# Kernel tuning notes

Measured on AMD Instinct MI355X. Metric: run time of the kernel, lower is better.

## Reference

```python
import jax, jax.numpy as jnp
import numpy as np

B, L, E, H = 128, 256, 256, 512


def setup_inputs() -> dict:
    key = jax.random.key(0)
    ks = jax.random.split(key, 16)
    s = 0.02
    return {
        "embedded_inputs": jax.random.normal(ks[0], (B, L, E), jnp.float32),
        "decoder_input": jax.random.normal(ks[1], (B, E), jnp.float32),
        "dec_h": jax.random.normal(ks[2], (B, H), jnp.float32),
        "dec_c": jax.random.normal(ks[3], (B, H), jnp.float32),
        "context": jax.random.normal(ks[4], (B, L, H), jnp.float32),
        # Decoder params
        "W_i2h": jax.random.normal(ks[5], (4 * H, E), jnp.float32) * s,
        "b_i2h": jnp.zeros((4 * H,), jnp.float32),
        "W_h2h": jax.random.normal(ks[6], (4 * H, H), jnp.float32) * s,
        "b_h2h": jnp.zeros((4 * H,), jnp.float32),
        "W_out": jax.random.normal(ks[7], (H, 2 * H), jnp.float32) * s,
        "b_out": jnp.zeros((H,), jnp.float32),
        # Attention params
        "W_inp": jax.random.normal(ks[8], (H, H), jnp.float32) * s,
        "b_inp": jnp.zeros((H,), jnp.float32),
        "W_ctx": jax.random.normal(ks[9], (H, H), jnp.float32) * s,  # Conv1d(k=1) kernel squeezed
        "b_ctx": jnp.zeros((H,), jnp.float32),
        "V": jax.random.uniform(ks[10], (H,), jnp.float32, -1.0, 1.0),
    }


def reference(embedded_inputs, decoder_input, dec_h, dec_c, context,
              W_i2h, b_i2h, W_h2h, b_h2h, W_out, b_out,
              W_inp, b_inp, W_ctx, b_ctx, V):
    # Precompute projected context: Conv1d(k=1) == per-position linear. ctx: [B, H, L]
    ctx = jnp.einsum("blh,gh->bgl", context, W_ctx) + b_ctx[None, :, None]
    seq_len = embedded_inputs.shape[1]

    def step(carry, _):
        x, h, c, mask = carry
        gates = x @ W_i2h.T + b_i2h + h @ W_h2h.T + b_h2h
        i, f, g, o = jnp.split(gates, 4, axis=1)
        c_t = jax.nn.sigmoid(f) * c + jax.nn.sigmoid(i) * jnp.tanh(g)
        h_t = jax.nn.sigmoid(o) * jnp.tanh(c_t)
        # attention
        inp = h_t @ W_inp.T + b_inp                              # [B, H]
        scores = jnp.einsum("h,bhl->bl", V, jnp.tanh(inp[:, :, None] + ctx))
        att = jnp.where(mask == 0, -jnp.inf, scores)
        alpha = jax.nn.softmax(att, axis=-1)                     # [B, L]
        hidden = jnp.einsum("bhl,bl->bh", ctx, alpha)
        h_new = jnp.tanh(jnp.concatenate([hidden, h_t], axis=1) @ W_out.T + b_out)
        # pointer selection
        idx = jnp.argmax(alpha * mask, axis=1)                   # [B]
        one_hot = jax.nn.one_hot(idx, seq_len, dtype=mask.dtype)
        mask_new = mask * (1.0 - one_hot)
        next_x = jnp.take_along_axis(embedded_inputs, idx[:, None, None], axis=1)[:, 0, :]
        return (next_x, h_new, c_t, mask_new), (alpha, idx)

    mask0 = jnp.ones((embedded_inputs.shape[0], seq_len), jnp.float32)
    (x_f, h_f, c_f, _), (alphas, ptrs) = jax.lax.scan(
        step, (decoder_input, dec_h, dec_c, mask0), None, length=seq_len)
    outputs = jnp.transpose(alphas, (1, 0, 2))   # [B, L, L]
    pointers = jnp.transpose(ptrs, (1, 0))       # [B, L]
    return outputs, pointers, h_f, c_f
```

## Files before the change

### kernel.cpp

```cpp
#include <hip/hip_runtime.h>

#define B 128
#define L 256
#define E 256
#define H 512
#define NBLK 256
#define NTHR 512

typedef float f4 __attribute__((ext_vector_type(4)));

#define WS_CTX 0u
#define WS_HT  18874368u
#define WS_HH  18939904u
#define WS_HID 19005440u
#define WS_INP 19071232u
#define WS_XT  19136768u
#define WS_FLG 19169536u

#define OUT_ALPHA 0u
#define OUT_PTR   8388608u
#define OUT_H     8421376u
#define OUT_C     8486912u

#define L2E 1.4426950408889634f

__device__ __forceinline__ float fast_rcp(float x) { return __builtin_amdgcn_rcpf(x); }

__device__ __forceinline__ float ftanh(float x) {
  float e = exp2f(x * (2.0f * L2E));
  return 1.0f - 2.0f * fast_rcp(e + 1.0f);
}
__device__ __forceinline__ float fsig(float x) {
  float e = exp2f(-x * L2E);
  return fast_rcp(1.0f + e);
}

#define CLD1(v0, p0)                                                          \
  asm volatile("global_load_dwordx4 %0, %1, off sc0 sc1\n\t"                  \
               "s_waitcnt vmcnt(0)"                                           \
               : "=&v"(v0) : "v"(p0) : "memory")

#define CLD2(va, pa)                                                          \
  asm volatile("global_load_dwordx4 %0, %2, off sc0 sc1\n\t"                  \
               "global_load_dwordx4 %1, %3, off sc0 sc1\n\t"                  \
               "s_waitcnt vmcnt(0)"                                           \
               : "=&v"(va[0]), "=&v"(va[1])                                   \
               : "v"(pa[0]), "v"(pa[1]) : "memory")

#define CLD4(va, pa)                                                          \
  asm volatile("global_load_dwordx4 %0, %4, off sc0 sc1\n\t"                  \
               "global_load_dwordx4 %1, %5, off sc0 sc1\n\t"                  \
               "global_load_dwordx4 %2, %6, off sc0 sc1\n\t"                  \
               "global_load_dwordx4 %3, %7, off sc0 sc1\n\t"                  \
               "s_waitcnt vmcnt(0)"                                           \
               : "=&v"(va[0]), "=&v"(va[1]), "=&v"(va[2]), "=&v"(va[3])       \
               : "v"(pa[0]), "v"(pa[1]), "v"(pa[2]), "v"(pa[3]) : "memory")

#define CLD6(va, pa)                                                          \
  asm volatile("global_load_dwordx4 %0, %6, off sc0 sc1\n\t"                  \
               "global_load_dwordx4 %1, %7, off sc0 sc1\n\t"                  \
               "global_load_dwordx4 %2, %8, off sc0 sc1\n\t"                  \
               "global_load_dwordx4 %3, %9, off sc0 sc1\n\t"                  \
               "global_load_dwordx4 %4, %10, off sc0 sc1\n\t"                 \
               "global_load_dwordx4 %5, %11, off sc0 sc1\n\t"                 \
               "s_waitcnt vmcnt(0)"                                           \
               : "=&v"(va[0]), "=&v"(va[1]), "=&v"(va[2]), "=&v"(va[3]),      \
                 "=&v"(va[4]), "=&v"(va[5])                                   \
               : "v"(pa[0]), "v"(pa[1]), "v"(pa[2]), "v"(pa[3]),              \
                 "v"(pa[4]), "v"(pa[5]) : "memory")

#define CST4_1(p0, v0)                                                        \
  asm volatile("global_store_dwordx4 %0, %1, off sc0 sc1\n\t"                 \
               "s_waitcnt expcnt(0)"                                          \
               :: "v"(p0), "v"(v0) : "memory")

__device__ __forceinline__ void gbar(unsigned* flags, unsigned tgt) {
  asm volatile("s_waitcnt vmcnt(0) lgkmcnt(0) expcnt(0)" ::: "memory");
  __syncthreads();
  if (threadIdx.x == 0) {
    unsigned* p = flags + blockIdx.x;
    asm volatile("global_store_dword %0, %1, off sc0 sc1" :: "v"(p), "v"(tgt) : "memory");
  }
  if (blockIdx.x == 0) {
    if (threadIdx.x < 64) {
      const unsigned* fp = flags + threadIdx.x * 4;
      for (;;) {
        unsigned f0, f1, f2, f3;
        asm volatile("global_load_dwordx4 v[20:23], %4, off sc0 sc1\n\t"
                     "s_waitcnt vmcnt(0)\n\t"
                     "v_mov_b32 %0, v20\n\t"
                     "v_mov_b32 %1, v21\n\t"
                     "v_mov_b32 %2, v22\n\t"
                     "v_mov_b32 %3, v23"
                     : "=v"(f0), "=v"(f1), "=v"(f2), "=v"(f3)
                     : "v"(fp) : "memory", "v20", "v21", "v22", "v23");
        bool ok = (f0 >= tgt) && (f1 >= tgt) && (f2 >= tgt) && (f3 >= tgt);
        if (__all(ok)) break;
        __builtin_amdgcn_s_sleep(1);
      }
    }
    __syncthreads();
    if (threadIdx.x == 0) {
      unsigned* gp = flags + 320;
      asm volatile("global_store_dword %0, %1, off sc0 sc1" :: "v"(gp), "v"(tgt) : "memory");
    }
  } else {
    if (threadIdx.x == 0) {
      const unsigned* gp = flags + 320;
      for (;;) {
        unsigned g;
        asm volatile("global_load_dword %0, %1, off sc0 sc1\n\ts_waitcnt vmcnt(0)"
                     : "=&v"(g) : "v"(gp) : "memory");
        if (g >= tgt) break;
        __builtin_amdgcn_s_sleep(4);
      }
    }
  }
  __syncthreads();
}

__global__ __launch_bounds__(256) void k_ctx(const float* __restrict__ context,
                                             const float* __restrict__ Wc,
                                             const float* __restrict__ bc,
                                             float* __restrict__ ws) {
  __shared__ float a_lds[64][33];
  __shared__ float b_lds[32][68];
  int t = threadIdx.x;
  int m0 = blockIdx.x * 64;
  int n0 = blockIdx.y * 64;
  int tx = t & 15, ty = t >> 4;
  float acc[4][4] = {};
  for (int kc = 0; kc < 16; ++kc) {
    int k0 = kc * 32;
    __syncthreads();
#pragma unroll
    for (int i = 0; i < 2; ++i) {
      int f40 = t + i * 256;
      int mm = f40 >> 3;
      int k4 = (f40 & 7) * 4;
      float4 v = *(const float4*)&context[(size_t)(m0 + mm) * H + k0 + k4];
      a_lds[mm][k4] = v.x; a_lds[mm][k4 + 1] = v.y; a_lds[mm][k4 + 2] = v.z; a_lds[mm][k4 + 3] = v.w;
    }
#pragma unroll
    for (int i = 0; i < 2; ++i) {
      int f40 = t + i * 256;
      int nn = f40 >> 3;
      int k4 = (f40 & 7) * 4;
      float4 v = *(const float4*)&Wc[(size_t)(n0 + nn) * H + k0 + k4];
      b_lds[k4][nn] = v.x; b_lds[k4 + 1][nn] = v.y; b_lds[k4 + 2][nn] = v.z; b_lds[k4 + 3][nn] = v.w;
    }
    __syncthreads();
#pragma unroll
    for (int kk = 0; kk < 32; ++kk) {
      float4 bv = *(const float4*)&b_lds[kk][tx * 4];
      float a0 = a_lds[ty * 4 + 0][kk], a1 = a_lds[ty * 4 + 1][kk];
      float a2 = a_lds[ty * 4 + 2][kk], a3 = a_lds[ty * 4 + 3][kk];
      acc[0][0] += a0 * bv.x; acc[0][1] += a0 * bv.y; acc[0][2] += a0 * bv.z; acc[0][3] += a0 * bv.w;
      acc[1][0] += a1 * bv.x; acc[1][1] += a1 * bv.y; acc[1][2] += a1 * bv.z; acc[1][3] += a1 * bv.w;
      acc[2][0] += a2 * bv.x; acc[2][1] += a2 * bv.y; acc[2][2] += a2 * bv.z; acc[2][3] += a2 * bv.w;
      acc[3][0] += a3 * bv.x; acc[3][1] += a3 * bv.y; acc[3][2] += a3 * bv.z; acc[3][3] += a3 * bv.w;
    }
  }
  float b0v = bc[n0 + tx * 4], b1v = bc[n0 + tx * 4 + 1], b2v = bc[n0 + tx * 4 + 2], b3v = bc[n0 + tx * 4 + 3];
#pragma unroll
  for (int i = 0; i < 4; ++i) {
    size_t o = WS_CTX + (size_t)(m0 + ty * 4 + i) * H + n0 + tx * 4;
    float4 v; v.x = acc[i][0] + b0v; v.y = acc[i][1] + b1v; v.z = acc[i][2] + b2v; v.w = acc[i][3] + b3v;
    *(float4*)&ws[o] = v;
  }
}

__global__ __launch_bounds__(256) void k_init(const float* __restrict__ dec_h,
                                              const float* __restrict__ dec_in,
                                              float* __restrict__ ws) {
  int flat = blockIdx.x * 256 + threadIdx.x;
  if (flat < 65536) {
    ws[WS_HH + flat] = dec_h[flat];
  } else if (flat < 98304) {
    ws[WS_XT + (flat - 65536)] = dec_in[flat - 65536];
  } else if (flat < 98816) {
    ((unsigned*)(ws + WS_FLG))[flat - 98304] = 0u;
  }
}

__global__ __launch_bounds__(512, 1) void k_main(
    const float* __restrict__ Wi2h, const float* __restrict__ bi2h,
    const float* __restrict__ Wh2h, const float* __restrict__ bh2h,
    const float* __restrict__ Wout, const float* __restrict__ bout,
    const float* __restrict__ Winp, const float* __restrict__ binp,
    const float* __restrict__ Vv,   const float* __restrict__ emb,
    const float* __restrict__ dec_c,
    float* __restrict__ ws,         float* __restrict__ out) {
  __shared__ float s_act[13504];
  __shared__ float s_maskP[256];
  __shared__ float s_mw[8], s_dw[8];
  __shared__ float s_red[4];
  __shared__ int   s_redi[4];
  __shared__ int   s_wc[4], s_wb[4];
  __shared__ int   s_mi, s_cnt;

  unsigned* flags = (unsigned*)(ws + WS_FLG);
  const int bid = blockIdx.x;
  const int t = threadIdx.x;
  const int wv = t >> 6, ln = t & 63;
  unsigned tgt = 0;

  float creg = 0.f;

  if (bid < 128 && t < 256) s_maskP[t] = 1.0f;
  __syncthreads();

  for (int step = 0; step < L; ++step) {
    {
      const int jt = bid >> 3, bt = bid & 7;
      const int u0 = jt * 16, b0 = bt * 16;
      float* sact = s_act;
      float* sg   = s_act + 12352;
      f4 va[6]; const float* pa[6]; int sb[6], sq[6];
#pragma unroll
      for (int it = 0; it < 6; ++it) {
        unsigned c = (unsigned)(t + it * 512);
        int bl = (int)(c / 192u);
        int kq = (int)(c - (unsigned)bl * 192u);
        int kg = kq * 4;
        sb[it] = bl; sq[it] = kq;
        pa[it] = (kg < 256) ? ws + WS_XT + (size_t)(b0 + bl) * 256 + kg
                            : ws + WS_HH + (size_t)(b0 + bl) * 512 + (kg - 256);
      }
      CLD6(va, pa);
      __builtin_amdgcn_sched_barrier(0);
#pragma unroll
      for (int it = 0; it < 6; ++it) *(f4*)&sact[sb[it] * 772 + sq[it] * 4] = va[it];
      __syncthreads();

      const int jj = t >> 4, bb = t & 15;
      const int g = jj >> 3, up = (jj & 7) * 2;
      const int r0 = g * 512 + u0 + up;
      float a0 = 0.f, a1 = 0.f;
      {
        const float* w0 = Wi2h + (size_t)r0 * 256;
        const float* w1 = w0 + 256;
        const float* sa = sact + bb * 772;
#pragma unroll 8
        for (int k4 = 0; k4 < 64; ++k4) {
          float4 x = *(const float4*)&sa[k4 * 4];
          float4 p = *(const float4*)&w0[k4 * 4];
          float4 q = *(const float4*)&w1[k4 * 4];
          a0 += p.x * x.x + p.y * x.y + p.z * x.z + p.w * x.w;
          a1 += q.x * x.x + q.y * x.y + q.z * x.z + q.w * x.w;
        }
        const float* v0 = Wh2h + (size_t)r0 * 512;
        const float* v1 = v0 + 512;
        const float* shh = sa + 256;
#pragma unroll 8
        for (int k4 = 0; k4 < 128; ++k4) {
          float4 x = *(const float4*)&shh[k4 * 4];
          float4 p = *(const float4*)&v0[k4 * 4];
          float4 q = *(const float4*)&v1[k4 * 4];
          a0 += p.x * x.x + p.y * x.y + p.z * x.z + p.w * x.w;
          a1 += q.x * x.x + q.y * x.y + q.z * x.z + q.w * x.w;
        }
      }
      sg[(g * 16 + up) * 17 + bb]     = a0;
      sg[(g * 16 + up + 1) * 17 + bb] = a1;
      __syncthreads();
      if (t < 256) {
        const int uu = t >> 4, b2 = t & 15;
        const int j0 = u0 + uu;
        float si_ = sg[(     uu) * 17 + b2] + bi2h[       j0] + bh2h[       j0];
        float sf_ = sg[(16 + uu) * 17 + b2] + bi2h[ 512 + j0] + bh2h[ 512 + j0];
        float sg_ = sg[(32 + uu) * 17 + b2] + bi2h[1024 + j0] + bh2h[1024 + j0];
        float so_ = sg[(48 + uu) * 17 + b2] + bi2h[1536 + j0] + bh2h[1536 + j0];
        if (step == 0) creg = dec_c[(size_t)(b0 + b2) * 512 + j0];
        float cn = fsig(sf_) * creg + fsig(si_) * ftanh(sg_);
        creg = cn;
        float htv = fsig(so_) * ftanh(cn);
        s_act[b2 * 17 + uu] = htv;
        if (step == L - 1) out[OUT_C + (size_t)(b0 + b2) * 512 + j0] = cn;
      }
      __syncthreads();
      if (t < 64) {
        const int b2 = t >> 2, q = t & 3;
        f4 hv;
        hv[0] = s_act[b2 * 17 + q * 4 + 0];
        hv[1] = s_act[b2 * 17 + q * 4 + 1];
        hv[2] = s_act[b2 * 17 + q * 4 + 2];
        hv[3] = s_act[b2 * 17 + q * 4 + 3];
        float* hp = ws + WS_HT + (size_t)(b0 + b2) * 512 + u0 + q * 4;
        CST4_1(hp, hv);
      }
    }
    ++tgt; gbar(flags, tgt);

    {
      const int gt = bid >> 4, bt = bid & 15;
      const int g0 = gt * 32, b0 = bt * 8;
      float* si = s_act;
      float* stmp = s_act + 4128;
      f4 va[2]; const float* pa[2];
#pragma unroll
      for (int it = 0; it < 2; ++it) {
        int c = t + it * 512;
        int bl = c >> 7, kq = c & 127;
        pa[it] = ws + WS_HT + (size_t)(b0 + bl) * 512 + kq * 4;
      }
      CLD2(va, pa);
      __builtin_amdgcn_sched_barrier(0);
#pragma unroll
      for (int it = 0; it < 2; ++it) {
        int c = t + it * 512;
        int bl = c >> 7, kq = c & 127;
        *(f4*)&si[bl * 516 + kq * 4] = va[it];
      }
      __syncthreads();
      if (t < 256) {
        const int gl = t >> 3, bb = t & 7;
        const float* w = Winp + (size_t)(g0 + gl) * 512;
        const float* sa = si + bb * 516;
        float acc = 0.f;
#pragma unroll 8
        for (int k4 = 0; k4 < 128; ++k4) {
          float4 ww = *(const float4*)&w[k4 * 4];
          float4 xx = *(const float4*)&sa[k4 * 4];
          acc += ww.x * xx.x + ww.y * xx.y + ww.z * xx.z + ww.w * xx.w;
        }
        stmp[bb * 33 + gl] = acc + binp[g0 + gl];
      }
      __syncthreads();
      if (t < 64) {
        const int bb = t >> 3, q = t & 7;
        f4 v;
        v[0] = stmp[bb * 33 + q * 4 + 0];
        v[1] = stmp[bb * 33 + q * 4 + 1];
        v[2] = stmp[bb * 33 + q * 4 + 2];
        v[3] = stmp[bb * 33 + q * 4 + 3];
        float* p = ws + WS_INP + (size_t)(b0 + bb) * 512 + g0 + q * 4;
        CST4_1(p, v);
      }
    }
    ++tgt; gbar(flags, tgt);

    if (bid < 128) {
      const int b = bid;
      float* s_inp  = s_act;
      float* s_sc   = s_act + 512;
      int*   s_li   = (int*)(s_act + 768);
      float* s_hidp = s_act + 1024;
      float* s_out  = s_act + 5120;
      if (t < 128) {
        f4 v;
        const float* p = ws + WS_INP + (size_t)b * 512 + t * 4;
        CLD1(v, p);
        *(f4*)&s_inp[t * 4] = v;
      }
      __syncthreads();
      const int d0 = ln * 8;
      float inp8[8], v8[8];
#pragma unroll
      for (int i = 0; i < 8; ++i) { inp8[i] = s_inp[d0 + i]; v8[i] = Vv[d0 + i]; }
      bool validl = (t < 256) && (s_maskP[t] != 0.f);
      unsigned long long bal = __ballot(validl);
      if (t < 256 && (t & 63) == 0) s_wc[t >> 6] = (int)__popcll(bal);
      __syncthreads();
      if (t == 0) {
        int base = 0;
#pragma unroll
        for (int i = 0; i < 4; ++i) { s_wb[i] = base; base += s_wc[i]; }
        s_cnt = base;
      }
      __syncthreads();
      if (validl) {
        int idx = s_wb[t >> 6] + (int)__popcll(bal & ((1ull << (t & 63)) - 1ull));
        s_li[idx] = t;
      }
      __syncthreads();
      const int cnt = s_cnt;
      float m = -INFINITY, den = 0.f;
      float hid[8] = {0, 0, 0, 0, 0, 0, 0, 0};
      {
        int slot = wv;
        int l = 0; f4 c0 = {0, 0, 0, 0}, c1 = c0;
        if (slot < cnt) {
          l = s_li[slot];
          const float* cp = ws + WS_CTX + ((size_t)(b * 256 + l) * 512) + d0;
          c0 = *(const f4*)cp; c1 = *(const f4*)(cp + 4);
        }
        while (slot < cnt) {
          const int nslot = slot + 8;
          int nl = 0; f4 n0 = {0, 0, 0, 0}, n1 = n0;
          if (nslot < cnt) {
            nl = s_li[nslot];
            const float* np = ws + WS_CTX + ((size_t)(b * 256 + nl) * 512) + d0;
            n0 = *(const f4*)np; n1 = *(const f4*)(np + 4);
          }
          float part = v8[0] * ftanh(inp8[0] + c0[0]) + v8[1] * ftanh(inp8[1] + c0[1])
                     + v8[2] * ftanh(inp8[2] + c0[2]) + v8[3] * ftanh(inp8[3] + c0[3])
                     + v8[4] * ftanh(inp8[4] + c1[0]) + v8[5] * ftanh(inp8[5] + c1[1])
                     + v8[6] * ftanh(inp8[6] + c1[2]) + v8[7] * ftanh(inp8[7] + c1[3]);
#pragma unroll
          for (int off = 32; off > 0; off >>= 1) part += __shfl_xor(part, off);
          if (ln == 0) s_sc[l] = part;
          float mn = fmaxf(m, part);
          float scale = exp2f((m - mn) * L2E);
          float e = exp2f((part - mn) * L2E);
          den = den * scale + e;
          hid[0] = hid[0] * scale + e * c0[0]; hid[1] = hid[1] * scale + e * c0[1];
          hid[2] = hid[2] * scale + e * c0[2]; hid[3] = hid[3] * scale + e * c0[3];
          hid[4] = hid[4] * scale + e * c1[0]; hid[5] = hid[5] * scale + e * c1[1];
          hid[6] = hid[6] * scale + e * c1[2]; hid[7] = hid[7] * scale + e * c1[3];
          m = mn;
          c0 = n0; c1 = n1; l = nl; slot = nslot;
        }
      }
      if (ln == 0) { s_mw[wv] = m; s_dw[wv] = den; }
      __syncthreads();
      float M = s_mw[0];
#pragma unroll
      for (int w = 1; w < 8; ++w) M = fmaxf(M, s_mw[w]);
      float D = 0.f;
#pragma unroll
      for (int w = 0; w < 8; ++w) D += s_dw[w] * exp2f((s_mw[w] - M) * L2E);
      float fac = exp2f((m - M) * L2E);
#pragma unroll
      for (int i = 0; i < 8; ++i) s_hidp[wv * 512 + d0 + i] = hid[i] * fac;
      __syncthreads();
      const float rD = 1.0f / D;
      {
        float hs = 0.f;
#pragma unroll
        for (int w = 0; w < 8; ++w) hs += s_hidp[w * 512 + t];
        s_out[t] = hs * rD;
      }
      float sc = 0.f; bool valid = false;
      if (t < 256) {
        valid = (s_maskP[t] != 0.f);
        sc = s_sc[t];
        float alpha = valid ? exp2f((sc - M) * L2E) * rD : 0.f;
        out[OUT_ALPHA + ((size_t)b * 256 + step) * 256 + t] = alpha;
        float bs = valid ? sc : -INFINITY;
        int bi = t;
#pragma unroll
        for (int off = 32; off > 0; off >>= 1) {
          float os = __shfl_down(bs, off);
          int oi = __shfl_down(bi, off);
          if (os > bs || (os == bs && oi < bi)) { bs = os; bi = oi; }
        }
        if ((t & 63) == 0) { s_red[t >> 6] = bs; s_redi[t >> 6] = bi; }
      }
      __syncthreads();
      if (t == 0) {
        float mm = s_red[0]; int mi = s_redi[0];
#pragma unroll
        for (int w = 1; w < 4; ++w) {
          if (s_red[w] > mm || (s_red[w] == mm && s_redi[w] < mi)) { mm = s_red[w]; mi = s_redi[w]; }
        }
        s_mi = mi;
      }
      __syncthreads();
      const int mi = s_mi;
      if (t < 128) {
        f4 hv = *(const f4*)&s_out[t * 4];
        float* hp = ws + WS_HID + (size_t)b * 512 + t * 4;
        CST4_1(hp, hv);
      }
      if (t < 64) {
        float4 xv = *(const float4*)&emb[((size_t)b * 256 + mi) * 256 + t * 4];
        f4 xq; xq[0] = xv.x; xq[1] = xv.y; xq[2] = xv.z; xq[3] = xv.w;
        float* xp = ws + WS_XT + (size_t)b * 256 + t * 4;
        CST4_1(xp, xq);
      }
      if (t == 0) {
        out[OUT_PTR + (size_t)b * 256 + step] = (float)mi;
        s_maskP[mi] = 0.f;
      }
    }
    ++tgt; gbar(flags, tgt);

    {
      const int rt = bid >> 4, bt = bid & 15;
      const int r0 = rt * 32, b0 = bt * 8;
      float* sh = s_act;
      float* stmp = s_act + 8224;
      f4 va[4]; const float* pa[4];
#pragma unroll
      for (int it = 0; it < 4; ++it) {
        int c = t + it * 512;
        int bl = c >> 8, kq = c & 255;
        int kg = kq * 4;
        pa[it] = (kg < 512) ? ws + WS_HID + (size_t)(b0 + bl) * 512 + kg
                            : ws + WS_HT + (size_t)(b0 + bl) * 512 + (kg - 512);
      }
      CLD4(va, pa);
      __builtin_amdgcn_sched_barrier(0);
#pragma unroll
      for (int it = 0; it < 4; ++it) {
        int c = t + it * 512;
        int bl = c >> 8, kq = c & 255;
        *(f4*)&sh[bl * 1028 + kq * 4] = va[it];
      }
      __syncthreads();
      if (t < 256) {
        const int rl = t >> 3, bb = t & 7;
        const float* w = Wout + (size_t)(r0 + rl) * 1024;
        const float* sa = sh + bb * 1028;
        float acc = 0.f;
#pragma unroll 8
        for (int k4 = 0; k4 < 256; ++k4) {
          float4 ww = *(const float4*)&w[k4 * 4];
          float4 xx = *(const float4*)&sa[k4 * 4];
          acc += ww.x * xx.x + ww.y * xx.y + ww.z * xx.z + ww.w * xx.w;
        }
        float h = ftanh(acc + bout[r0 + rl]);
        stmp[bb * 33 + rl] = h;
        if (step == L - 1) out[OUT_H + (size_t)(b0 + bb) * 512 + r0 + rl] = h;
      }
      __syncthreads();
      if (t < 64) {
        const int bb = t >> 3, q = t & 7;
        f4 v;
        v[0] = stmp[bb * 33 + q * 4 + 0];
        v[1] = stmp[bb * 33 + q * 4 + 1];
        v[2] = stmp[bb * 33 + q * 4 + 2];
        v[3] = stmp[bb * 33 + q * 4 + 3];
        float* p = ws + WS_HH + (size_t)(b0 + bb) * 512 + r0 + q * 4;
        CST4_1(p, v);
      }
    }
    ++tgt; gbar(flags, tgt);
  }
}

extern "C" void kernel_launch(void* const* d_in, const int* in_sizes, int n_in,
                              void* d_out, int out_size, void* d_ws, size_t ws_size,
                              hipStream_t stream) {
  (void)in_sizes; (void)n_in; (void)out_size; (void)ws_size;
  const float* emb    = (const float*)d_in[0];
  const float* dec_in = (const float*)d_in[1];
  const float* dec_h  = (const float*)d_in[2];
  const float* dec_c  = (const float*)d_in[3];
  const float* ctx_in = (const float*)d_in[4];
  const float* W_i2h  = (const float*)d_in[5];
  const float* b_i2h  = (const float*)d_in[6];
  const float* W_h2h  = (const float*)d_in[7];
  const float* b_h2h  = (const float*)d_in[8];
  const float* W_out  = (const float*)d_in[9];
  const float* b_out  = (const float*)d_in[10];
  const float* W_inp  = (const float*)d_in[11];
  const float* b_inp  = (const float*)d_in[12];
  const float* W_ctx  = (const float*)d_in[13];
  const float* b_ctx  = (const float*)d_in[14];
  const float* Vv     = (const float*)d_in[15];
  float* out = (float*)d_out;
  float* ws  = (float*)d_ws;

  k_ctx<<<dim3(512, 8), 256, 0, stream>>>(ctx_in, W_ctx, b_ctx, ws);
  k_init<<<386, 256, 0, stream>>>(dec_h, dec_in, ws);
  k_main<<<NBLK, NTHR, 0, stream>>>(W_i2h, b_i2h, W_h2h, b_h2h, W_out, b_out,
                                    W_inp, b_inp, Vv, emb, dec_c, ws, out);
}
```

Measured before the change: 18.97 ms.

## Pad barrier flags, remap block tiles per XCD, and unroll attention loop by four

Each block's grid-barrier flag now sits on its own padded slot, and the release flag is replicated eight times so waiters spread across copies selected by blockIdx&7. The waiter sleep interval is also shortened. Block-to-tile mappings in the three GEMM phases are permuted so blocks sharing bid&7 (likely the same XCD) work on neighbouring weight rows. The attention loop now handles four context positions per iteration with nontemporal prefetched loads and a batched online-softmax update, which cuts shuffle-reduction serialization but raises register pressure.

Result: faster. 16.53 ms (-12.9%).

```diff
diff --git a/kernel.cpp b/kernel.cpp
--- a/kernel.cpp
+++ b/kernel.cpp
@@ -78,41 +78,42 @@
   asm volatile("s_waitcnt vmcnt(0) lgkmcnt(0) expcnt(0)" ::: "memory");
   __syncthreads();
   if (threadIdx.x == 0) {
-    unsigned* p = flags + blockIdx.x;
+    unsigned* p = flags + blockIdx.x * 16;
     asm volatile("global_store_dword %0, %1, off sc0 sc1" :: "v"(p), "v"(tgt) : "memory");
   }
   if (blockIdx.x == 0) {
     if (threadIdx.x < 64) {
-      const unsigned* fp = flags + threadIdx.x * 4;
+      const unsigned* p0 = flags + (threadIdx.x * 4 + 0) * 16;
+      const unsigned* p1 = flags + (threadIdx.x * 4 + 1) * 16;
+      const unsigned* p2 = flags + (threadIdx.x * 4 + 2) * 16;
+      const unsigned* p3 = flags + (threadIdx.x * 4 + 3) * 16;
       for (;;) {
         unsigned f0, f1, f2, f3;
-        asm volatile("global_load_dwordx4 v[20:23], %4, off sc0 sc1\n\t"
-                     "s_waitcnt vmcnt(0)\n\t"
-                     "v_mov_b32 %0, v20\n\t"
-                     "v_mov_b32 %1, v21\n\t"
-                     "v_mov_b32 %2, v22\n\t"
-                     "v_mov_b32 %3, v23"
-                     : "=v"(f0), "=v"(f1), "=v"(f2), "=v"(f3)
-                     : "v"(fp) : "memory", "v20", "v21", "v22", "v23");
-        bool ok = (f0 >= tgt) && (f1 >= tgt) && (f2 >= tgt) && (f3 >= tgt);
-        if (__all(ok)) break;
+        asm volatile("global_load_dword %0, %4, off sc0 sc1\n\t"
+                     "global_load_dword %1, %5, off sc0 sc1\n\t"
+                     "global_load_dword %2, %6, off sc0 sc1\n\t"
+                     "global_load_dword %3, %7, off sc0 sc1\n\t"
+                     "s_waitcnt vmcnt(0)"
+                     : "=&v"(f0), "=&v"(f1), "=&v"(f2), "=&v"(f3)
+                     : "v"(p0), "v"(p1), "v"(p2), "v"(p3) : "memory");
+        if (__all(f0 >= tgt && f1 >= tgt && f2 >= tgt && f3 >= tgt)) break;
         __builtin_amdgcn_s_sleep(1);
       }
     }
     __syncthreads();
-    if (threadIdx.x == 0) {
-      unsigned* gp = flags + 320;
+    if (threadIdx.x < 8) {
+      unsigned* gp = flags + 4096 + threadIdx.x * 16;
       asm volatile("global_store_dword %0, %1, off sc0 sc1" :: "v"(gp), "v"(tgt) : "memory");
     }
   } else {
     if (threadIdx.x == 0) {
-      const unsigned* gp = flags + 320;
+      const unsigned* gp = flags + 4096 + (blockIdx.x & 7) * 16;
       for (;;) {
         unsigned g;
         asm volatile("global_load_dword %0, %1, off sc0 sc1\n\ts_waitcnt vmcnt(0)"
                      : "=&v"(g) : "v"(gp) : "memory");
         if (g >= tgt) break;
-        __builtin_amdgcn_s_sleep(4);
+        __builtin_amdgcn_s_sleep(2);
       }
     }
   }
@@ -178,7 +179,7 @@
     ws[WS_HH + flat] = dec_h[flat];
   } else if (flat < 98304) {
     ws[WS_XT + (flat - 65536)] = dec_in[flat - 65536];
-  } else if (flat < 98816) {
+  } else if (flat < 102528) {
     ((unsigned*)(ws + WS_FLG))[flat - 98304] = 0u;
   }
 }
@@ -212,7 +213,8 @@
 
   for (int step = 0; step < L; ++step) {
     {
-      const int jt = bid >> 3, bt = bid & 7;
+      const int jt = (bid & 7) * 4 + ((bid >> 3) & 3);
+      const int bt = bid >> 5;
       const int u0 = jt * 16, b0 = bt * 16;
       float* sact = s_act;
       float* sg   = s_act + 12352;
@@ -293,7 +295,8 @@
     ++tgt; gbar(flags, tgt);
 
     {
-      const int gt = bid >> 4, bt = bid & 15;
+      const int gt = (bid & 7) * 2 + ((bid >> 3) & 1);
+      const int bt = bid >> 4;
       const int g0 = gt * 32, b0 = bt * 8;
       float* si = s_act;
       float* stmp = s_act + 4128;
@@ -378,38 +381,102 @@
       float m = -INFINITY, den = 0.f;
       float hid[8] = {0, 0, 0, 0, 0, 0, 0, 0};
       {
-        int slot = wv;
-        int l = 0; f4 c0 = {0, 0, 0, 0}, c1 = c0;
-        if (slot < cnt) {
-          l = s_li[slot];
-          const float* cp = ws + WS_CTX + ((size_t)(b * 256 + l) * 512) + d0;
-          c0 = *(const f4*)cp; c1 = *(const f4*)(cp + 4);
-        }
-        while (slot < cnt) {
-          const int nslot = slot + 8;
-          int nl = 0; f4 n0 = {0, 0, 0, 0}, n1 = n0;
-          if (nslot < cnt) {
-            nl = s_li[nslot];
-            const float* np = ws + WS_CTX + ((size_t)(b * 256 + nl) * 512) + d0;
-            n0 = *(const f4*)np; n1 = *(const f4*)(np + 4);
+        f4 cur0a, cur0b, cur1a, cur1b, cur2a, cur2b, cur3a, cur3b;
+        int l0i, l1i, l2i, l3i;
+        int base = wv * 4;
+        {
+          int s0 = base, s1 = base + 1, s2 = base + 2, s3 = base + 3;
+          int a = (s0 < cnt) ? s_li[s0] : 0;  l0i = (s0 < cnt) ? a : -1;
+          int bb2 = (s1 < cnt) ? s_li[s1] : 0; l1i = (s1 < cnt) ? bb2 : -1;
+          int c = (s2 < cnt) ? s_li[s2] : 0;  l2i = (s2 < cnt) ? c : -1;
+          int d = (s3 < cnt) ? s_li[s3] : 0;  l3i = (s3 < cnt) ? d : -1;
+          const f4* p0 = (const f4*)(ws + WS_CTX + ((size_t)(b * 256 + a) * 512) + d0);
+          const f4* p1 = (const f4*)(ws + WS_CTX + ((size_t)(b * 256 + bb2) * 512) + d0);
+          const f4* p2 = (const f4*)(ws + WS_CTX + ((size_t)(b * 256 + c) * 512) + d0);
+          const f4* p3 = (const f4*)(ws + WS_CTX + ((size_t)(b * 256 + d) * 512) + d0);
+          cur0a = __builtin_nontemporal_load(p0); cur0b = __builtin_nontemporal_load(p0 + 1);
+          cur1a = __builtin_nontemporal_load(p1); cur1b = __builtin_nontemporal_load(p1 + 1);
+          cur2a = __builtin_nontemporal_load(p2); cur2b = __builtin_nontemporal_load(p2 + 1);
+          cur3a = __builtin_nontemporal_load(p3); cur3b = __builtin_nontemporal_load(p3 + 1);
+        }
+        for (; base < cnt; base += 32) {
+          f4 n0a, n0b, n1a, n1b, n2a, n2b, n3a, n3b;
+          int nl0, nl1, nl2, nl3;
+          {
+            int s0 = base + 32, s1 = base + 33, s2 = base + 34, s3 = base + 35;
+            int a = (s0 < cnt) ? s_li[s0] : 0;  nl0 = (s0 < cnt) ? a : -1;
+            int bb2 = (s1 < cnt) ? s_li[s1] : 0; nl1 = (s1 < cnt) ? bb2 : -1;
+            int c = (s2 < cnt) ? s_li[s2] : 0;  nl2 = (s2 < cnt) ? c : -1;
+            int d = (s3 < cnt) ? s_li[s3] : 0;  nl3 = (s3 < cnt) ? d : -1;
+            const f4* p0 = (const f4*)(ws + WS_CTX + ((size_t)(b * 256 + a) * 512) + d0);
+            const f4* p1 = (const f4*)(ws + WS_CTX + ((size_t)(b * 256 + bb2) * 512) + d0);
+            const f4* p2 = (const f4*)(ws + WS_CTX + ((size_t)(b * 256 + c) * 512) + d0);
+            const f4* p3 = (const f4*)(ws + WS_CTX + ((size_t)(b * 256 + d) * 512) + d0);
+            n0a = __builtin_nontemporal_load(p0); n0b = __builtin_nontemporal_load(p0 + 1);
+            n1a = __builtin_nontemporal_load(p1); n1b = __builtin_nontemporal_load(p1 + 1);
+            n2a = __builtin_nontemporal_load(p2); n2b = __builtin_nontemporal_load(p2 + 1);
+            n3a = __builtin_nontemporal_load(p3); n3b = __builtin_nontemporal_load(p3 + 1);
           }
-          float part = v8[0] * ftanh(inp8[0] + c0[0]) + v8[1] * ftanh(inp8[1] + c0[1])
-                     + v8[2] * ftanh(inp8[2] + c0[2]) + v8[3] * ftanh(inp8[3] + c0[3])
-                     + v8[4] * ftanh(inp8[4] + c1[0]) + v8[5] * ftanh(inp8[5] + c1[1])
-                     + v8[6] * ftanh(inp8[6] + c1[2]) + v8[7] * ftanh(inp8[7] + c1[3]);
-#pragma unroll
-          for (int off = 32; off > 0; off >>= 1) part += __shfl_xor(part, off);
-          if (ln == 0) s_sc[l] = part;
-          float mn = fmaxf(m, part);
+          float sv0, sv1, sv2, sv3;
+          {
+            float part = v8[0] * ftanh(inp8[0] + cur0a[0]) + v8[1] * ftanh(inp8[1] + cur0a[1])
+                       + v8[2] * ftanh(inp8[2] + cur0a[2]) + v8[3] * ftanh(inp8[3] + cur0a[3])
+                       + v8[4] * ftanh(inp8[4] + cur0b[0]) + v8[5] * ftanh(inp8[5] + cur0b[1])
+                       + v8[6] * ftanh(inp8[6] + cur0b[2]) + v8[7] * ftanh(inp8[7] + cur0b[3]);
+#pragma unroll
+            for (int off = 32; off > 0; off >>= 1) part += __shfl_xor(part, off);
+            if (l0i >= 0 && ln == 0) s_sc[l0i] = part;
+            sv0 = (l0i >= 0) ? part : -INFINITY;
+          }
+          {
+            float part = v8[0] * ftanh(inp8[0] + cur1a[0]) + v8[1] * ftanh(inp8[1] + cur1a[1])
+                       + v8[2] * ftanh(inp8[2] + cur1a[2]) + v8[3] * ftanh(inp8[3] + cur1a[3])
+                       + v8[4] * ftanh(inp8[4] + cur1b[0]) + v8[5] * ftanh(inp8[5] + cur1b[1])
+                       + v8[6] * ftanh(inp8[6] + cur1b[2]) + v8[7] * ftanh(inp8[7] + cur1b[3]);
+#pragma unroll
+            for (int off = 32; off > 0; off >>= 1) part += __shfl_xor(part, off);
+            if (l1i >= 0 && ln == 0) s_sc[l1i] = part;
+            sv1 = (l1i >= 0) ? part : -INFINITY;
+          }
+          {
+            float part = v8[0] * ftanh(inp8[0] + cur2a[0]) + v8[1] * ftanh(inp8[1] + cur2a[1])
+                       + v8[2] * ftanh(inp8[2] + cur2a[2]) + v8[3] * ftanh(inp8[3] + cur2a[3])
+                       + v8[4] * ftanh(inp8[4] + cur2b[0]) + v8[5] * ftanh(inp8[5] + cur2b[1])
+                       + v8[6] * ftanh(inp8[6] + cur2b[2]) + v8[7] * ftanh(inp8[7] + cur2b[3]);
+#pragma unroll
+            for (int off = 32; off > 0; off >>= 1) part += __shfl_xor(part, off);
+            if (l2i >= 0 && ln == 0) s_sc[l2i] = part;
+            sv2 = (l2i >= 0) ? part : -INFINITY;
+          }
+          {
+            float part = v8[0] * ftanh(inp8[0] + cur3a[0]) + v8[1] * ftanh(inp8[1] + cur3a[1])
+                       + v8[2] * ftanh(inp8[2] + cur3a[2]) + v8[3] * ftanh(inp8[3] + cur3a[3])
+                       + v8[4] * ftanh(inp8[4] + cur3b[0]) + v8[5] * ftanh(inp8[5] + cur3b[1])
+                       + v8[6] * ftanh(inp8[6] + cur3b[2]) + v8[7] * ftanh(inp8[7] + cur3b[3]);
+#pragma unroll
+            for (int off = 32; off > 0; off >>= 1) part += __shfl_xor(part, off);
+            if (l3i >= 0 && ln == 0) s_sc[l3i] = part;
+            sv3 = (l3i >= 0) ? part : -INFINITY;
+          }
+          float mn = fmaxf(m, fmaxf(fmaxf(sv0, sv1), fmaxf(sv2, sv3)));
           float scale = exp2f((m - mn) * L2E);
-          float e = exp2f((part - mn) * L2E);
-          den = den * scale + e;
-          hid[0] = hid[0] * scale + e * c0[0]; hid[1] = hid[1] * scale + e * c0[1];
-          hid[2] = hid[2] * scale + e * c0[2]; hid[3] = hid[3] * scale + e * c0[3];
-          hid[4] = hid[4] * scale + e * c1[0]; hid[5] = hid[5] * scale + e * c1[1];
-          hid[6] = hid[6] * scale + e * c1[2]; hid[7] = hid[7] * scale + e * c1[3];
+          float e0 = exp2f((sv0 - mn) * L2E);
+          float e1 = exp2f((sv1 - mn) * L2E);
+          float e2 = exp2f((sv2 - mn) * L2E);
+          float e3 = exp2f((sv3 - mn) * L2E);
+          den = den * scale + ((e0 + e1) + (e2 + e3));
+          hid[0] = hid[0] * scale + e0 * cur0a[0] + e1 * cur1a[0] + e2 * cur2a[0] + e3 * cur3a[0];
+          hid[1] = hid[1] * scale + e0 * cur0a[1] + e1 * cur1a[1] + e2 * cur2a[1] + e3 * cur3a[1];
+          hid[2] = hid[2] * scale + e0 * cur0a[2] + e1 * cur1a[2] + e2 * cur2a[2] + e3 * cur3a[2];
+          hid[3] = hid[3] * scale + e0 * cur0a[3] + e1 * cur1a[3] + e2 * cur2a[3] + e3 * cur3a[3];
+          hid[4] = hid[4] * scale + e0 * cur0b[0] + e1 * cur1b[0] + e2 * cur2b[0] + e3 * cur3b[0];
+          hid[5] = hid[5] * scale + e0 * cur0b[1] + e1 * cur1b[1] + e2 * cur2b[1] + e3 * cur3b[1];
+          hid[6] = hid[6] * scale + e0 * cur0b[2] + e1 * cur1b[2] + e2 * cur2b[2] + e3 * cur3b[2];
+          hid[7] = hid[7] * scale + e0 * cur0b[3] + e1 * cur1b[3] + e2 * cur2b[3] + e3 * cur3b[3];
           m = mn;
-          c0 = n0; c1 = n1; l = nl; slot = nslot;
+          cur0a = n0a; cur0b = n0b; cur1a = n1a; cur1b = n1b;
+          cur2a = n2a; cur2b = n2b; cur3a = n3a; cur3b = n3b;
+          l0i = nl0; l1i = nl1; l2i = nl2; l3i = nl3;
         }
       }
       if (ln == 0) { s_mw[wv] = m; s_dw[wv] = den; }
@@ -477,7 +544,8 @@
     ++tgt; gbar(flags, tgt);
 
     {
-      const int rt = bid >> 4, bt = bid & 15;
+      const int rt = (bid & 7) * 2 + ((bid >> 3) & 1);
+      const int bt = bid >> 4;
       const int r0 = rt * 32, b0 = bt * 8;
       float* sh = s_act;
       float* stmp = s_act + 8224;
@@ -554,7 +622,7 @@
   float* ws  = (float*)d_ws;
 
   k_ctx<<<dim3(512, 8), 256, 0, stream>>>(ctx_in, W_ctx, b_ctx, ws);
-  k_init<<<386, 256, 0, stream>>>(dec_h, dec_in, ws);
+  k_init<<<401, 256, 0, stream>>>(dec_h, dec_in, ws);
   k_main<<<NBLK, NTHR, 0, stream>>>(W_i2h, b_i2h, W_h2h, b_h2h, W_out, b_out,
                                     W_inp, b_inp, Vv, emb, dec_c, ws, out);
 }
```
